# Optimization experiments

Hardware: AMD Instinct MI355X
Metric: run time of the kernel (lower is better)

The kernel has to match this reference:

```python
import jax, jax.numpy as jnp
import numpy as np

B, S, D, H, DFF = 4, 2048, 1024, 16, 4096
DK = D // H
EPS = 1e-6


def setup_inputs() -> dict:
    key = jax.random.key(0)
    ks = jax.random.split(key, 8)
    s = 0.02
    return {
        "x": jax.random.normal(ks[0], (B, S, D), jnp.float32),
        "src_mask": jnp.ones((B, 1, 1, S), jnp.int32),
        "w_q": jax.random.normal(ks[1], (D, D), jnp.float32) * s,
        "w_k": jax.random.normal(ks[2], (D, D), jnp.float32) * s,
        "w_v": jax.random.normal(ks[3], (D, D), jnp.float32) * s,
        "w_o": jax.random.normal(ks[4], (D, D), jnp.float32) * s,
        "w1": jax.random.normal(ks[5], (DFF, D), jnp.float32) * s,
        "b1": jnp.zeros((DFF,), jnp.float32),
        "w2": jax.random.normal(ks[6], (D, DFF), jnp.float32) * s,
        "b2": jnp.zeros((D,), jnp.float32),
        "gamma1": jnp.ones((1,), jnp.float32),
        "beta1": jnp.zeros((1,), jnp.float32),
        "gamma2": jnp.ones((1,), jnp.float32),
        "beta2": jnp.zeros((1,), jnp.float32),
    }


def layernorm(x, gamma, beta):
    # matches torch source: unbiased std (ddof=1), eps added to std, scalar gamma/beta
    mean = jnp.mean(x, axis=-1, keepdims=True)
    std = jnp.std(x, axis=-1, keepdims=True, ddof=1)
    return gamma * (x - mean) / (std + EPS) + beta


def mha(x, w_q, w_k, w_v, w_o):
    # Linear(bias=False): y = x @ W.T
    q = (x @ w_q.T).reshape(B, S, H, DK).transpose(0, 2, 1, 3)  # [B,H,S,DK]
    k = (x @ w_k.T).reshape(B, S, H, DK).transpose(0, 2, 1, 3)
    v = (x @ w_v.T).reshape(B, S, H, DK).transpose(0, 2, 1, 3)
    scores = jnp.einsum('bhqd,bhkd->bhqk', q, k) / np.float32(np.sqrt(DK))
    # NOTE: source calls attention.masked_fill(...) without assigning the result,
    # so the mask has no effect; faithfully replicated (mask unused).
    attn = jax.nn.softmax(scores, axis=-1)
    ctx = jnp.einsum('bhqk,bhkd->bhqd', attn, v)  # [B,H,S,DK]
    ctx = ctx.transpose(0, 2, 1, 3).reshape(B, S, D)
    return ctx @ w_o.T


def ffn(x, w1, b1, w2, b2):
    return jax.nn.relu(x @ w1.T + b1) @ w2.T + b2


def reference(x, src_mask, w_q, w_k, w_v, w_o, w1, b1, w2, b2,
              gamma1, beta1, gamma2, beta2):
    # pre-norm residual blocks; dropout is identity in eval
    x = x + mha(layernorm(x, gamma1, beta1), w_q, w_k, w_v, w_o)
    x = x + ffn(layernorm(x, gamma2, beta2), w1, b1, w2, b2)
    return x
```

## Files before the change

### kernel.cpp

```cpp
#include <hip/hip_runtime.h>
#include <hip/hip_bf16.h>

#define DEV static __device__ __forceinline__

typedef unsigned short u16;
typedef float fp32x4 __attribute__((ext_vector_type(4)));
typedef short bf16x8 __attribute__((ext_vector_type(8)));
typedef short bf16x4 __attribute__((ext_vector_type(4)));

DEV float bf2f(u16 u) { return __uint_as_float(((unsigned)u) << 16); }
DEV u16 f2bf(float f) {
  unsigned x = __float_as_uint(f);
  x += 0x7fffu + ((x >> 16) & 1u);
  return (u16)(x >> 16);
}

DEV unsigned cvt_pk_bf16(float a, float b) {
  unsigned r;
  asm("v_cvt_pk_bf16_f32 %0, %1, %2" : "=v"(r) : "v"(a), "v"(b));
  return r;
}

DEV void gload_lds16(const void* g, void* l) {
  __builtin_amdgcn_global_load_lds(
      (__attribute__((address_space(1))) void*)(unsigned long long)g,
      (__attribute__((address_space(3))) void*)(unsigned int)(unsigned long long)l,
      16, 0, 0);
}

__global__ __launch_bounds__(256) void cvt_all(
    const float* __restrict__ wq, const float* __restrict__ wk,
    const float* __restrict__ wv, const float* __restrict__ wo,
    const float* __restrict__ w1, const float* __restrict__ w2,
    u16* __restrict__ dst) {
  const size_t i = (size_t)blockIdx.x * 256 + threadIdx.x;
  const size_t e = i * 4;
  const float* src;
  size_t off;
  const size_t M1 = 1u << 20;
  if (e < M1) { src = wq; off = e; }
  else if (e < 2 * M1) { src = wk; off = e - M1; }
  else if (e < 3 * M1) { src = wv; off = e - 2 * M1; }
  else if (e < 4 * M1) { src = wo; off = e - 3 * M1; }
  else if (e < 8 * M1) { src = w1; off = e - 4 * M1; }
  else { src = w2; off = e - 8 * M1; }
  const fp32x4 v = *(const fp32x4*)(src + off);
  bf16x4 o;
#pragma unroll
  for (int j = 0; j < 4; j++) o[j] = (short)f2bf(v[j]);
  ((bf16x4*)dst)[i] = o;
}

__global__ __launch_bounds__(256) void ln_kernel(const float* __restrict__ x,
                                                 u16* __restrict__ y,
                                                 const float* __restrict__ gamma,
                                                 const float* __restrict__ beta) {
  const int row = blockIdx.x;
  const int t = threadIdx.x;
  const fp32x4 v = ((const fp32x4*)(x + (size_t)row * 1024))[t];
  float s = v[0] + v[1] + v[2] + v[3];
  float ss = v[0] * v[0] + v[1] * v[1] + v[2] * v[2] + v[3] * v[3];
#pragma unroll
  for (int o = 32; o > 0; o >>= 1) {
    s += __shfl_down(s, o);
    ss += __shfl_down(ss, o);
  }
  __shared__ float rs[4], rss[4];
  const int w = t >> 6;
  if ((t & 63) == 0) { rs[w] = s; rss[w] = ss; }
  __syncthreads();
  const float S = rs[0] + rs[1] + rs[2] + rs[3];
  const float SS = rss[0] + rss[1] + rss[2] + rss[3];
  const float mean = S * (1.0f / 1024.0f);
  const float var = fmaxf((SS - 1024.0f * mean * mean) * (1.0f / 1023.0f), 0.0f);
  const float sc = gamma[0] / (sqrtf(var) + 1e-6f);
  const float be = beta[0];
  bf16x4 o;
#pragma unroll
  for (int j = 0; j < 4; j++) o[j] = (short)f2bf((v[j] - mean) * sc + be);
  ((bf16x4*)(y + (size_t)row * 1024))[t] = o;
}

template <int EPI>
__global__ __launch_bounds__(256, 2) void gemm_bt(
    const u16* __restrict__ A, const u16* __restrict__ W, u16* __restrict__ Cb,
    float* __restrict__ Cf, const float* __restrict__ bias,
    const float* __restrict__ resid, int M, int N, int K,
    u16* __restrict__ CbK, u16* __restrict__ CbV) {
  __shared__ u16 sA[128 * 32];
  __shared__ u16 sB[128 * 32];
  const int t = threadIdx.x;
  const int lane = t & 63;
  const int w = t >> 6;
  const int wr = (w >> 1) * 64;
  const int wc = (w & 1) * 64;
  const int lr = lane & 15;
  const int hi = lane >> 4;

  const int nwgx = gridDim.x;
  const int orig = blockIdx.y * nwgx + blockIdx.x;
  const int cpx = (nwgx * gridDim.y) >> 3;
  const int logical = (orig & 7) * cpx + (orig >> 3);
  const int bx = logical % nwgx, by = logical / nwgx;

  const u16* gA = A + (size_t)(by * 128 + (t >> 2)) * K + (t & 3) * 8;
  const u16* gB = W + (size_t)(bx * 128 + (t >> 2)) * K + (t & 3) * 8;
  const size_t rstep = (size_t)64 * K;
  u16* lA = &sA[t * 8];
  u16* lB = &sB[t * 8];

  const fp32x4 zero4 = {0.f, 0.f, 0.f, 0.f};
  fp32x4 acc[4][4];
#pragma unroll
  for (int i = 0; i < 4; i++)
#pragma unroll
    for (int j = 0; j < 4; j++) acc[i][j] = zero4;

  for (int k0 = 0; k0 < K; k0 += 32) {
    gload_lds16(gA, lA);
    gload_lds16(gA + rstep, lA + 2048);
    gload_lds16(gB, lB);
    gload_lds16(gB + rstep, lB + 2048);
    gA += 32;
    gB += 32;
    __syncthreads();
    bf16x8 af[4], bfr[4];
#pragma unroll
    for (int i = 0; i < 4; i++)
      af[i] = *(const bf16x8*)&sA[(wr + i * 16 + lr) * 32 + hi * 8];
#pragma unroll
    for (int j = 0; j < 4; j++)
      bfr[j] = *(const bf16x8*)&sB[(wc + j * 16 + lr) * 32 + hi * 8];
#pragma unroll
    for (int i = 0; i < 4; i++)
#pragma unroll
      for (int j = 0; j < 4; j++)
        acc[i][j] =
            __builtin_amdgcn_mfma_f32_16x16x32_bf16(af[i], bfr[j], acc[i][j], 0, 0, 0);
    __syncthreads();
  }

  const int row0 = by * 128 + wr + hi * 4;
  const int col0 = bx * 128 + wc + lr;

  if constexpr (EPI == 4) {
    if (col0 < 2048) {
      u16* qkvDst = (col0 >> 10) ? CbK : Cb;
      const int colL0 = col0 & 1023;
#pragma unroll
      for (int i = 0; i < 4; i++)
#pragma unroll
        for (int r = 0; r < 4; r++) {
          const size_t row = (size_t)(row0 + i * 16 + r);
#pragma unroll
          for (int j = 0; j < 4; j++)
            qkvDst[row * 1024 + colL0 + j * 16] = f2bf(acc[i][j][r]);
        }
    } else {
      __shared__ __attribute__((aligned(16))) u16 sT[2][64 * 72];
#pragma unroll
      for (int ph = 0; ph < 2; ++ph) {
        __syncthreads();
        if ((w >> 1) == ph) {
          u16* R = sT[w & 1];
#pragma unroll
          for (int j = 0; j < 4; j++) {
            const int ci = j * 16 + lr;
            const int X = (ci ^ (ci >> 3)) & 7;
#pragma unroll
            for (int i = 0; i < 4; i++)
#pragma unroll
              for (int r = 0; r < 4; r++) {
                const int ri = i * 16 + hi * 4 + r;
                R[ci * 72 + ((((ri >> 3) ^ X) << 3) | (ri & 7))] =
                    f2bf(acc[i][j][r]);
              }
          }
        }
        __syncthreads();
        if ((w >> 1) == ph) {
          const u16* R = sT[w & 1];
          const int ci = lane;
          const int X = (ci ^ (ci >> 3)) & 7;
          const int h = (bx - 16) * 2 + (w & 1);
          const int bidx = by >> 4;
          const int sb_base = (by & 15) * 128 + (w >> 1) * 64;
          u16* vdst = CbV + ((size_t)((bidx * 16 + h) * 64 + ci)) * 2048 + sb_base;
#pragma unroll
          for (int ch = 0; ch < 8; ch++) {
            bf16x8 vv = *(const bf16x8*)&R[ci * 72 + ((ch ^ X) << 3)];
            *(bf16x8*)(vdst + ch * 8) = vv;
          }
        }
      }
    }
    return;
  }

  float bj[4] = {0.f, 0.f, 0.f, 0.f};
  if (EPI == 1 || EPI == 3) {
#pragma unroll
    for (int j = 0; j < 4; j++) bj[j] = bias[col0 + j * 16];
  }
#pragma unroll
  for (int i = 0; i < 4; i++) {
#pragma unroll
    for (int r = 0; r < 4; r++) {
      const size_t row = (size_t)(row0 + i * 16 + r);
#pragma unroll
      for (int j = 0; j < 4; j++) {
        const int col = col0 + j * 16;
        float v = acc[i][j][r];
        if (EPI == 1) v = fmaxf(v + bj[j], 0.f);
        if (EPI == 3) v += bj[j];
        if (EPI >= 2) {
          v += resid[row * N + col];
          Cf[row * N + col] = v;
        } else {
          Cb[row * N + col] = f2bf(v);
        }
      }
    }
  }
}

DEV int swz(int row, int chunk) { return row * 64 + ((chunk ^ (row & 7)) << 3); }

__global__ __launch_bounds__(256, 2) void attn_kernel(const u16* __restrict__ Q,
                                                      const u16* __restrict__ K,
                                                      const u16* __restrict__ VT,
                                                      u16* __restrict__ O) {
  const int orig = blockIdx.x + 32 * (blockIdx.y + 16 * blockIdx.z);
  const int logical = (orig & 7) * 256 + (orig >> 3);
  const int qt = logical & 31;
  const int h = (logical >> 5) & 15;
  const int b = logical >> 9;

  const int t = threadIdx.x, lane = t & 63, w = t >> 6;
  const int lr = lane & 15, hi = lane >> 4;

  __shared__ u16 sK[64 * 64];
  __shared__ u16 sVT[64 * 64];
  __shared__ u16 sQP[64 * 64];

  const size_t base = ((size_t)b * 2048) * 1024 + (size_t)h * 64;
  const size_t vbase = (((size_t)b * 16 + h) * 64) * 2048;
  const int r = t >> 2, c0 = (t & 3) * 16;
  const int wch = (t & 3) * 2;

  {
    const float qs = 0.125f * 1.44269504f;
    const u16* src = Q + base + (size_t)(qt * 64 + r) * 1024 + c0;
    bf16x8 u0 = *(const bf16x8*)src;
    bf16x8 u1 = *(const bf16x8*)(src + 8);
    union { unsigned u[4]; bf16x8 v; } q0, q1;
#pragma unroll
    for (int j = 0; j < 4; j++)
      q0.u[j] = cvt_pk_bf16(bf2f((u16)u0[2 * j]) * qs, bf2f((u16)u0[2 * j + 1]) * qs);
#pragma unroll
    for (int j = 0; j < 4; j++)
      q1.u[j] = cvt_pk_bf16(bf2f((u16)u1[2 * j]) * qs, bf2f((u16)u1[2 * j + 1]) * qs);
    *(bf16x8*)&sQP[swz(r, wch)] = q0.v;
    *(bf16x8*)&sQP[swz(r, wch + 1)] = q1.v;
  }
  __syncthreads();
  const int qrow = w * 16 + lr;
  bf16x8 qreg0 = *(const bf16x8*)&sQP[swz(qrow, hi)];
  bf16x8 qreg1 = *(const bf16x8*)&sQP[swz(qrow, 4 + hi)];

  bf16x8 kA, kB, vA, vB;
  {
    const u16* ks = K + base + (size_t)r * 1024 + c0;
    kA = *(const bf16x8*)ks;
    kB = *(const bf16x8*)(ks + 8);
    const u16* vs = VT + vbase + (size_t)r * 2048 + c0;
    vA = *(const bf16x8*)vs;
    vB = *(const bf16x8*)(vs + 8);
  }

  const fp32x4 zero4 = {0.f, 0.f, 0.f, 0.f};
  fp32x4 onT[4];
#pragma unroll
  for (int df = 0; df < 4; df++) onT[df] = zero4;
  float mrun = -1e30f, lrun = 0.f;

  for (int kt = 0; kt < 32; ++kt) {
    __syncthreads();
    *(bf16x8*)&sK[swz(r, wch)] = kA;
    *(bf16x8*)&sK[swz(r, wch + 1)] = kB;
    *(bf16x8*)&sVT[swz(r, wch)] = vA;
    *(bf16x8*)&sVT[swz(r, wch + 1)] = vB;
    __syncthreads();
    if (kt < 31) {
      const u16* kn = K + base + (size_t)((kt + 1) * 64 + r) * 1024 + c0;
      kA = *(const bf16x8*)kn;
      kB = *(const bf16x8*)(kn + 8);
      const u16* vn = VT + vbase + (size_t)r * 2048 + (kt + 1) * 64 + c0;
      vA = *(const bf16x8*)vn;
      vB = *(const bf16x8*)(vn + 8);
    }

    fp32x4 sc[4];
    __builtin_amdgcn_s_setprio(1);
#pragma unroll
    for (int kk = 0; kk < 4; kk++) {
      fp32x4 a = zero4;
      bf16x8 kf0 = *(const bf16x8*)&sK[swz(kk * 16 + lr, hi)];
      bf16x8 kf1 = *(const bf16x8*)&sK[swz(kk * 16 + lr, 4 + hi)];
      a = __builtin_amdgcn_mfma_f32_16x16x32_bf16(kf0, qreg0, a, 0, 0, 0);
      a = __builtin_amdgcn_mfma_f32_16x16x32_bf16(kf1, qreg1, a, 0, 0, 0);
      sc[kk] = a;
    }
    __builtin_amdgcn_s_setprio(0);

    float m0 = fmaxf(fmaxf(sc[0][0], sc[0][1]), fmaxf(sc[0][2], sc[0][3]));
    float m1 = fmaxf(fmaxf(sc[1][0], sc[1][1]), fmaxf(sc[1][2], sc[1][3]));
    float m2 = fmaxf(fmaxf(sc[2][0], sc[2][1]), fmaxf(sc[2][2], sc[2][3]));
    float m3 = fmaxf(fmaxf(sc[3][0], sc[3][1]), fmaxf(sc[3][2], sc[3][3]));
    float mloc = fmaxf(fmaxf(m0, m1), fmaxf(m2, m3));
    mloc = fmaxf(mloc, __shfl_xor(mloc, 16));
    mloc = fmaxf(mloc, __shfl_xor(mloc, 32));
    if (!__all(mloc - mrun <= 11.0f)) {
      const float mnew = fmaxf(mrun, mloc);
      const float alpha = exp2f(mrun - mnew);
      lrun *= alpha;
#pragma unroll
      for (int df = 0; df < 4; df++) onT[df] *= alpha;
      mrun = mnew;
    }
#pragma unroll
    for (int kk = 0; kk < 4; kk++) {
      float p0 = exp2f(sc[kk][0] - mrun), p1 = exp2f(sc[kk][1] - mrun);
      float p2 = exp2f(sc[kk][2] - mrun), p3 = exp2f(sc[kk][3] - mrun);
      lrun += (p0 + p1) + (p2 + p3);
      uint2 pk = {cvt_pk_bf16(p0, p1), cvt_pk_bf16(p2, p3)};
      *(uint2*)&sQP[swz(qrow, 2 * kk + (hi >> 1)) + (hi & 1) * 4] = pk;
    }

    __builtin_amdgcn_s_setprio(1);
#pragma unroll
    for (int df = 0; df < 4; df++) {
#pragma unroll
      for (int ks = 0; ks < 2; ks++) {
        bf16x8 vf = *(const bf16x8*)&sVT[swz(df * 16 + lr, ks * 4 + hi)];
        bf16x8 pf = *(const bf16x8*)&sQP[swz(qrow, ks * 4 + hi)];
        onT[df] = __builtin_amdgcn_mfma_f32_16x16x32_bf16(vf, pf, onT[df], 0, 0, 0);
      }
    }
    __builtin_amdgcn_s_setprio(0);
  }

  lrun += __shfl_xor(lrun, 16);
  lrun += __shfl_xor(lrun, 32);
  const float invl = 1.0f / lrun;
  u16* dst = O + base + (size_t)(qt * 64 + qrow) * 1024;
#pragma unroll
  for (int df = 0; df < 4; df++) {
    uint2 o2 = {cvt_pk_bf16(onT[df][0] * invl, onT[df][1] * invl),
                cvt_pk_bf16(onT[df][2] * invl, onT[df][3] * invl)};
    *(uint2*)&dst[df * 16 + hi * 4] = o2;
  }
}

extern "C" void kernel_launch(void* const* d_in, const int* in_sizes, int n_in,
                              void* d_out, int out_size, void* d_ws, size_t ws_size,
                              hipStream_t stream) {
  const float* x = (const float*)d_in[0];
  const float* wq = (const float*)d_in[2];
  const float* wk = (const float*)d_in[3];
  const float* wv = (const float*)d_in[4];
  const float* wo = (const float*)d_in[5];
  const float* w1 = (const float*)d_in[6];
  const float* b1 = (const float*)d_in[7];
  const float* w2 = (const float*)d_in[8];
  const float* b2 = (const float*)d_in[9];
  const float* g1 = (const float*)d_in[10];
  const float* be1 = (const float*)d_in[11];
  const float* g2 = (const float*)d_in[12];
  const float* be2 = (const float*)d_in[13];
  float* out = (float*)d_out;

  const size_t MB = 1024ull * 1024ull;
  char* ws = (char*)d_ws;
  if (ws_size < 136 * MB) return;

  u16* wqkv = (u16*)(ws + 0 * MB);
  u16* wob = (u16*)(ws + 6 * MB);
  u16* w1b = (u16*)(ws + 8 * MB);
  u16* w2b = (u16*)(ws + 16 * MB);
  u16* Qb = (u16*)(ws + 24 * MB);
  u16* Kb = (u16*)(ws + 40 * MB);
  u16* VTb = (u16*)(ws + 56 * MB);
  u16* Ctx = (u16*)(ws + 72 * MB);
  u16* Hb = (u16*)(ws + 24 * MB);
  u16* Yb = (u16*)(ws + 88 * MB);
  float* X2 = (float*)(ws + 104 * MB);

  dim3 blk(256);

  cvt_all<<<12288, blk, 0, stream>>>(wq, wk, wv, wo, w1, w2, (u16*)ws);

  ln_kernel<<<8192, blk, 0, stream>>>(x, Yb, g1, be1);

  gemm_bt<4><<<dim3(24, 64), blk, 0, stream>>>(Yb, wqkv, Qb, nullptr, nullptr, nullptr,
                                               8192, 3072, 1024, Kb, VTb);

  attn_kernel<<<dim3(32, 16, 4), blk, 0, stream>>>(Qb, Kb, VTb, Ctx);

  gemm_bt<2><<<dim3(8, 64), blk, 0, stream>>>(Ctx, wob, nullptr, X2, nullptr, x, 8192,
                                              1024, 1024, nullptr, nullptr);

  ln_kernel<<<8192, blk, 0, stream>>>(X2, Yb, g2, be2);

  gemm_bt<1><<<dim3(32, 64), blk, 0, stream>>>(Yb, w1b, Hb, nullptr, b1, nullptr, 8192,
                                               4096, 1024, nullptr, nullptr);

  gemm_bt<3><<<dim3(8, 64), blk, 0, stream>>>(Hb, w2b, nullptr, out, b2, X2, 8192, 1024,
                                              4096, nullptr, nullptr);
}
```

Measured before the change: 440.3 us.

## Process two query tiles per attention block to reuse K/V tiles

```diff
diff --git a/kernel.cpp b/kernel.cpp
--- a/kernel.cpp
+++ b/kernel.cpp
@@ -230,11 +230,11 @@
                                                       const u16* __restrict__ K,
                                                       const u16* __restrict__ VT,
                                                       u16* __restrict__ O) {
-  const int orig = blockIdx.x + 32 * (blockIdx.y + 16 * blockIdx.z);
-  const int logical = (orig & 7) * 256 + (orig >> 3);
-  const int qt = logical & 31;
-  const int h = (logical >> 5) & 15;
-  const int b = logical >> 9;
+  const int orig = blockIdx.x + 16 * (blockIdx.y + 16 * blockIdx.z);
+  const int logical = (orig & 7) * 128 + (orig >> 3);
+  const int qt = logical & 15;
+  const int h = (logical >> 4) & 15;
+  const int b = logical >> 8;
 
   const int t = threadIdx.x, lane = t & 63, w = t >> 6;
   const int lr = lane & 15, hi = lane >> 4;
@@ -247,12 +247,14 @@
   const size_t vbase = (((size_t)b * 16 + h) * 64) * 2048;
   const int r = t >> 2, c0 = (t & 3) * 16;
   const int wch = (t & 3) * 2;
-
+  const int qrow = w * 16 + lr;
+  const float qs = 0.125f * 1.44269504f;
+
+  bf16x8 qA0, qA1, qB0, qB1;
   {
-    const float qs = 0.125f * 1.44269504f;
-    const u16* src = Q + base + (size_t)(qt * 64 + r) * 1024 + c0;
-    bf16x8 u0 = *(const bf16x8*)src;
-    bf16x8 u1 = *(const bf16x8*)(src + 8);
+    const u16* srcA = Q + base + (size_t)(qt * 64 + r) * 1024 + c0;
+    bf16x8 u0 = *(const bf16x8*)srcA;
+    bf16x8 u1 = *(const bf16x8*)(srcA + 8);
     union { unsigned u[4]; bf16x8 v; } q0, q1;
 #pragma unroll
     for (int j = 0; j < 4; j++)
@@ -262,11 +264,25 @@
       q1.u[j] = cvt_pk_bf16(bf2f((u16)u1[2 * j]) * qs, bf2f((u16)u1[2 * j + 1]) * qs);
     *(bf16x8*)&sQP[swz(r, wch)] = q0.v;
     *(bf16x8*)&sQP[swz(r, wch + 1)] = q1.v;
-  }
-  __syncthreads();
-  const int qrow = w * 16 + lr;
-  bf16x8 qreg0 = *(const bf16x8*)&sQP[swz(qrow, hi)];
-  bf16x8 qreg1 = *(const bf16x8*)&sQP[swz(qrow, 4 + hi)];
+    __syncthreads();
+    qA0 = *(const bf16x8*)&sQP[swz(qrow, hi)];
+    qA1 = *(const bf16x8*)&sQP[swz(qrow, 4 + hi)];
+    __syncthreads();
+    const u16* srcB = Q + base + (size_t)((qt + 16) * 64 + r) * 1024 + c0;
+    u0 = *(const bf16x8*)srcB;
+    u1 = *(const bf16x8*)(srcB + 8);
+#pragma unroll
+    for (int j = 0; j < 4; j++)
+      q0.u[j] = cvt_pk_bf16(bf2f((u16)u0[2 * j]) * qs, bf2f((u16)u0[2 * j + 1]) * qs);
+#pragma unroll
+    for (int j = 0; j < 4; j++)
+      q1.u[j] = cvt_pk_bf16(bf2f((u16)u1[2 * j]) * qs, bf2f((u16)u1[2 * j + 1]) * qs);
+    *(bf16x8*)&sQP[swz(r, wch)] = q0.v;
+    *(bf16x8*)&sQP[swz(r, wch + 1)] = q1.v;
+    __syncthreads();
+    qB0 = *(const bf16x8*)&sQP[swz(qrow, hi)];
+    qB1 = *(const bf16x8*)&sQP[swz(qrow, 4 + hi)];
+  }
 
   bf16x8 kA, kB, vA, vB;
   {
@@ -279,10 +295,11 @@
   }
 
   const fp32x4 zero4 = {0.f, 0.f, 0.f, 0.f};
-  fp32x4 onT[4];
-#pragma unroll
-  for (int df = 0; df < 4; df++) onT[df] = zero4;
-  float mrun = -1e30f, lrun = 0.f;
+  fp32x4 onTA[4], onTB[4];
+#pragma unroll
+  for (int df = 0; df < 4; df++) { onTA[df] = zero4; onTB[df] = zero4; }
+  float mrunA = -1e30f, lrunA = 0.f;
+  float mrunB = -1e30f, lrunB = 0.f;
 
   for (int kt = 0; kt < 32; ++kt) {
     __syncthreads();
@@ -307,58 +324,113 @@
       fp32x4 a = zero4;
       bf16x8 kf0 = *(const bf16x8*)&sK[swz(kk * 16 + lr, hi)];
       bf16x8 kf1 = *(const bf16x8*)&sK[swz(kk * 16 + lr, 4 + hi)];
-      a = __builtin_amdgcn_mfma_f32_16x16x32_bf16(kf0, qreg0, a, 0, 0, 0);
-      a = __builtin_amdgcn_mfma_f32_16x16x32_bf16(kf1, qreg1, a, 0, 0, 0);
+      a = __builtin_amdgcn_mfma_f32_16x16x32_bf16(kf0, qA0, a, 0, 0, 0);
+      a = __builtin_amdgcn_mfma_f32_16x16x32_bf16(kf1, qA1, a, 0, 0, 0);
       sc[kk] = a;
     }
     __builtin_amdgcn_s_setprio(0);
-
-    float m0 = fmaxf(fmaxf(sc[0][0], sc[0][1]), fmaxf(sc[0][2], sc[0][3]));
-    float m1 = fmaxf(fmaxf(sc[1][0], sc[1][1]), fmaxf(sc[1][2], sc[1][3]));
-    float m2 = fmaxf(fmaxf(sc[2][0], sc[2][1]), fmaxf(sc[2][2], sc[2][3]));
-    float m3 = fmaxf(fmaxf(sc[3][0], sc[3][1]), fmaxf(sc[3][2], sc[3][3]));
-    float mloc = fmaxf(fmaxf(m0, m1), fmaxf(m2, m3));
-    mloc = fmaxf(mloc, __shfl_xor(mloc, 16));
-    mloc = fmaxf(mloc, __shfl_xor(mloc, 32));
-    if (!__all(mloc - mrun <= 11.0f)) {
-      const float mnew = fmaxf(mrun, mloc);
-      const float alpha = exp2f(mrun - mnew);
-      lrun *= alpha;
-#pragma unroll
-      for (int df = 0; df < 4; df++) onT[df] *= alpha;
-      mrun = mnew;
-    }
+    {
+      float m0 = fmaxf(fmaxf(sc[0][0], sc[0][1]), fmaxf(sc[0][2], sc[0][3]));
+      float m1 = fmaxf(fmaxf(sc[1][0], sc[1][1]), fmaxf(sc[1][2], sc[1][3]));
+      float m2 = fmaxf(fmaxf(sc[2][0], sc[2][1]), fmaxf(sc[2][2], sc[2][3]));
+      float m3 = fmaxf(fmaxf(sc[3][0], sc[3][1]), fmaxf(sc[3][2], sc[3][3]));
+      float mloc = fmaxf(fmaxf(m0, m1), fmaxf(m2, m3));
+      mloc = fmaxf(mloc, __shfl_xor(mloc, 16));
+      mloc = fmaxf(mloc, __shfl_xor(mloc, 32));
+      if (!__all(mloc - mrunA <= 11.0f)) {
+        const float mnew = fmaxf(mrunA, mloc);
+        const float alpha = exp2f(mrunA - mnew);
+        lrunA *= alpha;
+#pragma unroll
+        for (int df = 0; df < 4; df++) onTA[df] *= alpha;
+        mrunA = mnew;
+      }
+#pragma unroll
+      for (int kk = 0; kk < 4; kk++) {
+        float p0 = exp2f(sc[kk][0] - mrunA), p1 = exp2f(sc[kk][1] - mrunA);
+        float p2 = exp2f(sc[kk][2] - mrunA), p3 = exp2f(sc[kk][3] - mrunA);
+        lrunA += (p0 + p1) + (p2 + p3);
+        uint2 pk = {cvt_pk_bf16(p0, p1), cvt_pk_bf16(p2, p3)};
+        *(uint2*)&sQP[swz(qrow, 2 * kk + (hi >> 1)) + (hi & 1) * 4] = pk;
+      }
+      __builtin_amdgcn_s_setprio(1);
+#pragma unroll
+      for (int df = 0; df < 4; df++) {
+#pragma unroll
+        for (int ks = 0; ks < 2; ks++) {
+          bf16x8 vf = *(const bf16x8*)&sVT[swz(df * 16 + lr, ks * 4 + hi)];
+          bf16x8 pf = *(const bf16x8*)&sQP[swz(qrow, ks * 4 + hi)];
+          onTA[df] = __builtin_amdgcn_mfma_f32_16x16x32_bf16(vf, pf, onTA[df], 0, 0, 0);
+        }
+      }
+      __builtin_amdgcn_s_setprio(0);
+    }
+
+    __builtin_amdgcn_s_setprio(1);
 #pragma unroll
     for (int kk = 0; kk < 4; kk++) {
-      float p0 = exp2f(sc[kk][0] - mrun), p1 = exp2f(sc[kk][1] - mrun);
-      float p2 = exp2f(sc[kk][2] - mrun), p3 = exp2f(sc[kk][3] - mrun);
-      lrun += (p0 + p1) + (p2 + p3);
-      uint2 pk = {cvt_pk_bf16(p0, p1), cvt_pk_bf16(p2, p3)};
-      *(uint2*)&sQP[swz(qrow, 2 * kk + (hi >> 1)) + (hi & 1) * 4] = pk;
-    }
-
-    __builtin_amdgcn_s_setprio(1);
-#pragma unroll
-    for (int df = 0; df < 4; df++) {
-#pragma unroll
-      for (int ks = 0; ks < 2; ks++) {
-        bf16x8 vf = *(const bf16x8*)&sVT[swz(df * 16 + lr, ks * 4 + hi)];
-        bf16x8 pf = *(const bf16x8*)&sQP[swz(qrow, ks * 4 + hi)];
-        onT[df] = __builtin_amdgcn_mfma_f32_16x16x32_bf16(vf, pf, onT[df], 0, 0, 0);
-      }
+      fp32x4 a = zero4;
+      bf16x8 kf0 = *(const bf16x8*)&sK[swz(kk * 16 + lr, hi)];
+      bf16x8 kf1 = *(const bf16x8*)&sK[swz(kk * 16 + lr, 4 + hi)];
+      a = __builtin_amdgcn_mfma_f32_16x16x32_bf16(kf0, qB0, a, 0, 0, 0);
+      a = __builtin_amdgcn_mfma_f32_16x16x32_bf16(kf1, qB1, a, 0, 0, 0);
+      sc[kk] = a;
     }
     __builtin_amdgcn_s_setprio(0);
-  }
-
-  lrun += __shfl_xor(lrun, 16);
-  lrun += __shfl_xor(lrun, 32);
-  const float invl = 1.0f / lrun;
-  u16* dst = O + base + (size_t)(qt * 64 + qrow) * 1024;
+    {
+      float m0 = fmaxf(fmaxf(sc[0][0], sc[0][1]), fmaxf(sc[0][2], sc[0][3]));
+      float m1 = fmaxf(fmaxf(sc[1][0], sc[1][1]), fmaxf(sc[1][2], sc[1][3]));
+      float m2 = fmaxf(fmaxf(sc[2][0], sc[2][1]), fmaxf(sc[2][2], sc[2][3]));
+      float m3 = fmaxf(fmaxf(sc[3][0], sc[3][1]), fmaxf(sc[3][2], sc[3][3]));
+      float mloc = fmaxf(fmaxf(m0, m1), fmaxf(m2, m3));
+      mloc = fmaxf(mloc, __shfl_xor(mloc, 16));
+      mloc = fmaxf(mloc, __shfl_xor(mloc, 32));
+      if (!__all(mloc - mrunB <= 11.0f)) {
+        const float mnew = fmaxf(mrunB, mloc);
+        const float alpha = exp2f(mrunB - mnew);
+        lrunB *= alpha;
+#pragma unroll
+        for (int df = 0; df < 4; df++) onTB[df] *= alpha;
+        mrunB = mnew;
+      }
+#pragma unroll
+      for (int kk = 0; kk < 4; kk++) {
+        float p0 = exp2f(sc[kk][0] - mrunB), p1 = exp2f(sc[kk][1] - mrunB);
+        float p2 = exp2f(sc[kk][2] - mrunB), p3 = exp2f(sc[kk][3] - mrunB);
+        lrunB += (p0 + p1) + (p2 + p3);
+        uint2 pk = {cvt_pk_bf16(p0, p1), cvt_pk_bf16(p2, p3)};
+        *(uint2*)&sQP[swz(qrow, 2 * kk + (hi >> 1)) + (hi & 1) * 4] = pk;
+      }
+      __builtin_amdgcn_s_setprio(1);
+#pragma unroll
+      for (int df = 0; df < 4; df++) {
+#pragma unroll
+        for (int ks = 0; ks < 2; ks++) {
+          bf16x8 vf = *(const bf16x8*)&sVT[swz(df * 16 + lr, ks * 4 + hi)];
+          bf16x8 pf = *(const bf16x8*)&sQP[swz(qrow, ks * 4 + hi)];
+          onTB[df] = __builtin_amdgcn_mfma_f32_16x16x32_bf16(vf, pf, onTB[df], 0, 0, 0);
+        }
+      }
+      __builtin_amdgcn_s_setprio(0);
+    }
+  }
+
+  lrunA += __shfl_xor(lrunA, 16);
+  lrunA += __shfl_xor(lrunA, 32);
+  lrunB += __shfl_xor(lrunB, 16);
+  lrunB += __shfl_xor(lrunB, 32);
+  const float invlA = 1.0f / lrunA;
+  const float invlB = 1.0f / lrunB;
+  u16* dstA = O + base + (size_t)(qt * 64 + qrow) * 1024;
+  u16* dstB = O + base + (size_t)((qt + 16) * 64 + qrow) * 1024;
 #pragma unroll
   for (int df = 0; df < 4; df++) {
-    uint2 o2 = {cvt_pk_bf16(onT[df][0] * invl, onT[df][1] * invl),
-                cvt_pk_bf16(onT[df][2] * invl, onT[df][3] * invl)};
-    *(uint2*)&dst[df * 16 + hi * 4] = o2;
+    uint2 oA = {cvt_pk_bf16(onTA[df][0] * invlA, onTA[df][1] * invlA),
+                cvt_pk_bf16(onTA[df][2] * invlA, onTA[df][3] * invlA)};
+    *(uint2*)&dstA[df * 16 + hi * 4] = oA;
+    uint2 oB = {cvt_pk_bf16(onTB[df][0] * invlB, onTB[df][1] * invlB),
+                cvt_pk_bf16(onTB[df][2] * invlB, onTB[df][3] * invlB)};
+    *(uint2*)&dstB[df * 16 + hi * 4] = oB;
   }
 }
 
@@ -405,7 +477,7 @@
   gemm_bt<4><<<dim3(24, 64), blk, 0, stream>>>(Yb, wqkv, Qb, nullptr, nullptr, nullptr,
                                                8192, 3072, 1024, Kb, VTb);
 
-  attn_kernel<<<dim3(32, 16, 4), blk, 0, stream>>>(Qb, Kb, VTb, Ctx);
+  attn_kernel<<<dim3(16, 16, 4), blk, 0, stream>>>(Qb, Kb, VTb, Ctx);
 
   gemm_bt<2><<<dim3(8, 64), blk, 0, stream>>>(Ctx, wob, nullptr, X2, nullptr, x, 8192,
                                               1024, 1024, nullptr, nullptr);
```

Result: no change. 444.1 us (+0.9%).
